# Kernel optimization log

Hardware: AMD Instinct MI355X
Metric: run time of the kernel (lower is better)

Reference implementation:

```python
import jax, jax.numpy as jnp
import numpy as np

IMG_W, IMG_H = 800, 800
OH, OW = 7, 7


def setup_inputs() -> dict:
    key = jax.random.key(0)
    k1, k2, k3 = jax.random.split(key, 3)
    feature_map = jax.random.normal(k1, (1, 256, 200, 200), dtype=jnp.float32)
    # boxes in image pixel coords, x1<=x2 and y1<=y2
    xs = jnp.sort(jax.random.uniform(k2, (1024, 2), dtype=jnp.float32) * (IMG_W - 1), axis=1)
    ys = jnp.sort(jax.random.uniform(k3, (1024, 2), dtype=jnp.float32) * (IMG_H - 1), axis=1)
    boxes = jnp.stack([xs[:, 0], ys[:, 0], xs[:, 1], ys[:, 1]], axis=1)
    return {"feature_map": feature_map, "boxes": boxes}


def reference(feature_map, boxes):
    # feature_map: [1, C, H, W]; boxes: [N, 4] (x1, y1, x2, y2) in image coords
    fm = feature_map[0]                      # [C, H, W]
    C, H, W = fm.shape
    scale = jnp.array([W / IMG_W, H / IMG_H, W / IMG_W, H / IMG_H], dtype=boxes.dtype)
    b = jnp.floor(boxes * scale).astype(jnp.int32)
    x1 = jnp.clip(b[:, 0], 0, W - 1)
    y1 = jnp.clip(b[:, 1], 0, H - 1)
    x2 = jnp.clip(b[:, 2] + 1, x1 + 1, W)    # exclusive end, clamped like torch slicing
    y2 = jnp.clip(b[:, 3] + 1, y1 + 1, H)
    rh = y2 - y1                             # [N]
    rw = x2 - x1
    # adaptive_avg_pool2d bin edges: start=floor(i*L/O), end=ceil((i+1)*L/O)
    i = jnp.arange(OH)
    j = jnp.arange(OW)
    rs = y1[:, None] + (i[None, :] * rh[:, None]) // OH                  # [N, OH]
    re = y1[:, None] + ((i[None, :] + 1) * rh[:, None] + OH - 1) // OH
    cs = x1[:, None] + (j[None, :] * rw[:, None]) // OW                  # [N, OW]
    ce = x1[:, None] + ((j[None, :] + 1) * rw[:, None] + OW - 1) // OW
    # integral image with zero row/col padding: ii[c, r, k] = sum fm[c, :r, :k]
    ii = jnp.pad(jnp.cumsum(jnp.cumsum(fm, axis=1), axis=2), ((0, 0), (1, 0), (1, 0)))

    def S(r, c):  # r: [N, OH], c: [N, OW] -> [N, C, OH, OW]
        return ii[:, r[:, :, None], c[:, None, :]].transpose(1, 0, 2, 3)

    total = S(re, ce) - S(rs, ce) - S(re, cs) + S(rs, cs)               # [N, C, OH, OW]
    area = ((re - rs)[:, :, None] * (ce - cs)[:, None, :]).astype(fm.dtype)  # [N, OH, OW]
    return total / area[:, None, :, :]
```

## Files before the change

### kernel.cpp

```cpp
#include <hip/hip_runtime.h>

#define C_CH  256
#define H_FM  200
#define W_FM  200
#define N_BOX 1024
#define OHp   7
#define OWp   7
#define NG    8
#define CG    32
#define WC    (W_FM * C_CH)
#define NCHUNK 25
#define CHROWS 8
#define GSTRIDE (H_FM * W_FM * CG)
#define HSTRIDE (W_FM * CG)
#define AUXG    (NCHUNK * HSTRIDE)


__global__ __launch_bounds__(256) void transpose_wscan_kernel(const float* __restrict__ fm,
                                                              float* __restrict__ T2) {
    __shared__ float tile[W_FM][CG + 1];
    __shared__ float tot[8][CG + 1];
    __shared__ float offE[8][CG + 1];
    const int t = threadIdx.x;
    const int h = blockIdx.x;
    const int g = blockIdx.y;
    const int c0 = g * CG;

    #pragma unroll
    for (int s = 0; s < 25; ++s) {
        int flat = s * 256 + t;
        int ci = flat / W_FM;
        int w  = flat - ci * W_FM;
        tile[w][ci] = fm[(size_t)(c0 + ci) * (H_FM * W_FM) + (size_t)h * W_FM + w];
    }
    __syncthreads();

    const int cg  = t & 31;
    const int chb = t >> 5;
    {
        float acc = 0.0f;
        #pragma unroll
        for (int s = 0; s < 25; ++s) {
            acc += tile[chb * 25 + s][cg];
            tile[chb * 25 + s][cg] = acc;
        }
        tot[chb][cg] = acc;
    }
    __syncthreads();

    {
        float off = 0.0f;
        #pragma unroll
        for (int k = 0; k < 8; ++k) {
            float v = tot[k][cg];
            if (k < chb) off += v;
        }
        offE[chb][cg] = off;
    }
    __syncthreads();

    float* dst = T2 + (size_t)g * GSTRIDE + (size_t)h * HSTRIDE;
    #pragma unroll
    for (int m = 0; m < 25; ++m) {
        int flat = m * 256 + t;
        int w  = flat >> 5;
        int cc = flat & 31;
        dst[flat] = tile[w][cc] + offE[w / 25][cc];
    }
}

__global__ __launch_bounds__(256) void colscan_chunk_kernel(float* __restrict__ T2,
                                                            float* __restrict__ aux2) {
    const int q4 = blockIdx.x * 256 + threadIdx.x;
    const int ch = blockIdx.y;
    const int g  = q4 / (HSTRIDE / 4);
    const int r4 = q4 - g * (HSTRIDE / 4);
    float4* p = (float4*)T2 + (size_t)g * (GSTRIDE / 4)
                            + (size_t)(ch * CHROWS) * (HSTRIDE / 4) + r4;
    float4 acc = make_float4(0.f, 0.f, 0.f, 0.f);
    #pragma unroll
    for (int k = 0; k < CHROWS; ++k) {
        float4 v = p[(size_t)k * (HSTRIDE / 4)];
        acc.x += v.x; acc.y += v.y; acc.z += v.z; acc.w += v.w;
        p[(size_t)k * (HSTRIDE / 4)] = acc;
    }
    ((float4*)aux2)[(size_t)g * (AUXG / 4) + (size_t)ch * (HSTRIDE / 4) + r4] = acc;
}

__global__ __launch_bounds__(256) void aux_scan_kernel(float* __restrict__ aux2) {
    const int idx = blockIdx.x * 256 + threadIdx.x;
    const int g   = idx / (HSTRIDE / 4);
    const int r4  = idx - g * (HSTRIDE / 4);
    float4* p = (float4*)aux2 + (size_t)g * (AUXG / 4) + r4;
    float4 acc = make_float4(0.f, 0.f, 0.f, 0.f);
    #pragma unroll
    for (int ch = 0; ch < NCHUNK; ++ch) {
        float4 v = p[(size_t)ch * (HSTRIDE / 4)];
        p[(size_t)ch * (HSTRIDE / 4)] = acc;
        acc.x += v.x; acc.y += v.y; acc.z += v.z; acc.w += v.w;
    }
}

__global__ __launch_bounds__(256) void pool5_kernel(const float* __restrict__ T2,
                                                    const float* __restrict__ aux2,
                                                    const float* __restrict__ boxes,
                                                    float* __restrict__ out) {
    __shared__ __align__(16) float lo[CG * 49];
    const int bx = blockIdx.x;
    const int n  = bx >> 3;
    const int g  = bx & 7;
    const int t  = threadIdx.x;
    const int cg = t & 31;
    const int islot = t >> 5;

    const float4 box = ((const float4*)boxes)[n];
    int b0 = (int)floorf(box.x * 0.25f);
    int b1 = (int)floorf(box.y * 0.25f);
    int b2 = (int)floorf(box.z * 0.25f);
    int b3 = (int)floorf(box.w * 0.25f);
    int x1 = min(max(b0, 0), W_FM - 1);
    int y1 = min(max(b1, 0), H_FM - 1);
    int x2 = min(max(b2 + 1, x1 + 1), W_FM);
    int y2 = min(max(b3 + 1, y1 + 1), H_FM);
    int rh = y2 - y1;
    int rw = x2 - x1;

    if (islot < OHp) {
        const int i  = islot;
        const int rt = y1 + (i * rh) / OHp;
        const int rb = y1 + ((i + 1) * rh + OHp - 1) / OHp;
        int colv[2 * OWp];
        #pragma unroll
        for (int j = 0; j < OWp; ++j) {
            colv[j]       = x1 + (j * rw) / OWp;
            colv[OWp + j] = x1 + ((j + 1) * rw + OWp - 1) / OWp;
        }
        const float* base = T2   + (size_t)g * GSTRIDE + cg;
        const float* abase = aux2 + (size_t)g * AUXG   + cg;
        const int ra  = max(rt - 1, 0) * W_FM;
        const int rbm = (rb - 1) * W_FM;
        const int ca  = (max(rt - 1, 0) >> 3) * W_FM;
        const int cb  = ((rb - 1) >> 3) * W_FM;
        float top[2 * OWp], bot[2 * OWp];
        #pragma unroll
        for (int k = 0; k < 2 * OWp; ++k) {
            const int kk = colv[k];
            const int ka = max(kk - 1, 0);
            float tv = base[(size_t)(ra  + ka) * CG] + abase[(size_t)(ca + ka) * CG];
            float bv = base[(size_t)(rbm + ka) * CG] + abase[(size_t)(cb + ka) * CG];
            top[k] = (rt > 0 && kk > 0) ? tv : 0.0f;
            bot[k] = (kk > 0)           ? bv : 0.0f;
        }
        const float rowspan = (float)(rb - rt);
        #pragma unroll
        for (int j = 0; j < OWp; ++j) {
            float total = (bot[OWp + j] - bot[j]) - (top[OWp + j] - top[j]);
            float area  = rowspan * (float)(colv[OWp + j] - colv[j]);
            lo[cg * 49 + i * OWp + j] = total / area;
        }
    }
    __syncthreads();

    float4* dst4 = (float4*)(out + (size_t)n * (C_CH * 49) + (size_t)g * (CG * 49));
    const float4* lo4 = (const float4*)lo;
    #pragma unroll
    for (int m = 0; m < 2; ++m) {
        int idx = m * 256 + t;
        if (idx < CG * 49 / 4) dst4[idx] = lo4[idx];
    }
}

__device__ __forceinline__ void box_edges(const float4 box, int i, int j,
                                          int& rs, int& re, int& cs, int& ce) {
    int b0 = (int)floorf(box.x * 0.25f);
    int b1 = (int)floorf(box.y * 0.25f);
    int b2 = (int)floorf(box.z * 0.25f);
    int b3 = (int)floorf(box.w * 0.25f);
    int x1 = min(max(b0, 0), W_FM - 1);
    int y1 = min(max(b1, 0), H_FM - 1);
    int x2 = min(max(b2 + 1, x1 + 1), W_FM);
    int y2 = min(max(b3 + 1, y1 + 1), H_FM);
    int rh = y2 - y1;
    int rw = x2 - x1;
    rs = y1 + (i * rh) / OHp;
    re = y1 + ((i + 1) * rh + OHp - 1) / OHp;
    cs = x1 + (j * rw) / OWp;
    ce = x1 + ((j + 1) * rw + OWp - 1) / OWp;
}

__global__ __launch_bounds__(256) void pool_direct_kernel(const float* __restrict__ fm,
                                                          const float* __restrict__ boxes,
                                                          float* __restrict__ out) {
    const int idx = blockIdx.x * 256 + threadIdx.x;
    const int j  = idx % OWp;
    const int t1 = idx / OWp;
    const int i  = t1 % OHp;
    const int t2 = t1 / OHp;
    const int c  = t2 % C_CH;
    const int n  = t2 / C_CH;

    const float4 box = ((const float4*)boxes)[n];
    int rs, re, cs, ce;
    box_edges(box, i, j, rs, re, cs, ce);

    const float* base = fm + (size_t)c * (H_FM * W_FM);
    float sum = 0.0f;
    for (int r = rs; r < re; ++r) {
        const float* rowp = base + (size_t)r * W_FM;
        for (int k = cs; k < ce; ++k) sum += rowp[k];
    }
    float area = (float)((re - rs) * (ce - cs));
    out[idx] = sum / area;
}

extern "C" void kernel_launch(void* const* d_in, const int* in_sizes, int n_in,
                              void* d_out, int out_size, void* d_ws, size_t ws_size,
                              hipStream_t stream) {
    const float* fm    = (const float*)d_in[0];
    const float* boxes = (const float*)d_in[1];
    float* out = (float*)d_out;

    const size_t tBytes   = (size_t)NG * GSTRIDE * sizeof(float);
    const size_t auxBytes = (size_t)NG * AUXG * sizeof(float);
    const int    total    = N_BOX * C_CH * OHp * OWp;
    const int    blocks   = total / 256;

    if (ws_size >= tBytes + auxBytes) {
        float* T2   = (float*)d_ws;
        float* aux2 = (float*)((char*)d_ws + tBytes);
        transpose_wscan_kernel<<<dim3(H_FM, NG), 256, 0, stream>>>(fm, T2);
        colscan_chunk_kernel<<<dim3(WC / 4 / 256, NCHUNK), 256, 0, stream>>>(T2, aux2);
        aux_scan_kernel<<<WC / 4 / 256, 256, 0, stream>>>(aux2);
        pool5_kernel<<<N_BOX * NG, 256, 0, stream>>>(T2, aux2, boxes, out);
    } else {
        pool_direct_kernel<<<blocks, 256, 0, stream>>>(fm, boxes, out);
    }
}
```

Measured before the change: 141.4 us.

## Fuse transpose, row scan and chunked column scan; stage pool corners in LDS

Merges the transpose/width-scan kernel with the chunked column-scan kernel. Each block walks 8 rows and carries running column sums in registers, so the extra read-modify-write pass over the integral buffer is gone. The pooling kernel now gathers all 14x14 corner values with vectorized loads into shared memory before combining them. The aux scan uses smaller blocks. The fused scan launches only 200 blocks with serialized row iterations, which may leave the GPU underoccupied.

```diff
diff --git a/kernel.cpp b/kernel.cpp
--- a/kernel.cpp
+++ b/kernel.cpp
@@ -16,79 +16,93 @@
 #define AUXG    (NCHUNK * HSTRIDE)
 
 
-__global__ __launch_bounds__(256) void transpose_wscan_kernel(const float* __restrict__ fm,
-                                                              float* __restrict__ T2) {
+__global__ __launch_bounds__(256) void fused_scan_kernel(const float* __restrict__ fm,
+                                                         float* __restrict__ T2,
+                                                         float* __restrict__ aux2) {
     __shared__ float tile[W_FM][CG + 1];
     __shared__ float tot[8][CG + 1];
     __shared__ float offE[8][CG + 1];
-    const int t = threadIdx.x;
-    const int h = blockIdx.x;
-    const int g = blockIdx.y;
-    const int c0 = g * CG;
-
-    #pragma unroll
-    for (int s = 0; s < 25; ++s) {
-        int flat = s * 256 + t;
-        int ci = flat / W_FM;
-        int w  = flat - ci * W_FM;
-        tile[w][ci] = fm[(size_t)(c0 + ci) * (H_FM * W_FM) + (size_t)h * W_FM + w];
-    }
-    __syncthreads();
-
+    const int t   = threadIdx.x;
+    const int chk = blockIdx.x;
+    const int g   = blockIdx.y;
+    const int c0  = g * CG;
+    const int h0  = chk * CHROWS;
     const int cg  = t & 31;
     const int chb = t >> 5;
-    {
-        float acc = 0.0f;
+
+    float4 acc[7];
+    #pragma unroll
+    for (int u = 0; u < 7; ++u) acc[u] = make_float4(0.f, 0.f, 0.f, 0.f);
+
+    const float* srcBase = fm + (size_t)c0 * (H_FM * W_FM);
+    float* dstBase = T2 + (size_t)g * GSTRIDE;
+
+    for (int hh = 0; hh < CHROWS; ++hh) {
+        const int h = h0 + hh;
+        const float* src = srcBase + (size_t)h * W_FM;
         #pragma unroll
-        for (int s = 0; s < 25; ++s) {
-            acc += tile[chb * 25 + s][cg];
-            tile[chb * 25 + s][cg] = acc;
-        }
-        tot[chb][cg] = acc;
-    }
-    __syncthreads();
-
-    {
-        float off = 0.0f;
+        for (int it = 0; it < 7; ++it) {
+            int item = it * 256 + t;
+            if (item < 1600) {
+                int ci = item / 50;
+                int w4 = item - ci * 50;
+                float4 v = *(const float4*)(src + (size_t)ci * (H_FM * W_FM) + w4 * 4);
+                tile[w4 * 4 + 0][ci] = v.x;
+                tile[w4 * 4 + 1][ci] = v.y;
+                tile[w4 * 4 + 2][ci] = v.z;
+                tile[w4 * 4 + 3][ci] = v.w;
+            }
+        }
+        __syncthreads();
+        {
+            float a = 0.f;
+            #pragma unroll
+            for (int s = 0; s < 25; ++s) {
+                a += tile[chb * 25 + s][cg];
+                tile[chb * 25 + s][cg] = a;
+            }
+            tot[chb][cg] = a;
+        }
+        __syncthreads();
+        {
+            float off = 0.f;
+            #pragma unroll
+            for (int k = 0; k < 8; ++k) {
+                float v = tot[k][cg];
+                if (k < chb) off += v;
+            }
+            offE[chb][cg] = off;
+        }
+        __syncthreads();
+        float* dst = dstBase + (size_t)h * HSTRIDE;
         #pragma unroll
-        for (int k = 0; k < 8; ++k) {
-            float v = tot[k][cg];
-            if (k < chb) off += v;
-        }
-        offE[chb][cg] = off;
-    }
-    __syncthreads();
-
-    float* dst = T2 + (size_t)g * GSTRIDE + (size_t)h * HSTRIDE;
-    #pragma unroll
-    for (int m = 0; m < 25; ++m) {
-        int flat = m * 256 + t;
-        int w  = flat >> 5;
-        int cc = flat & 31;
-        dst[flat] = tile[w][cc] + offE[w / 25][cc];
-    }
-}
-
-__global__ __launch_bounds__(256) void colscan_chunk_kernel(float* __restrict__ T2,
-                                                            float* __restrict__ aux2) {
-    const int q4 = blockIdx.x * 256 + threadIdx.x;
-    const int ch = blockIdx.y;
-    const int g  = q4 / (HSTRIDE / 4);
-    const int r4 = q4 - g * (HSTRIDE / 4);
-    float4* p = (float4*)T2 + (size_t)g * (GSTRIDE / 4)
-                            + (size_t)(ch * CHROWS) * (HSTRIDE / 4) + r4;
-    float4 acc = make_float4(0.f, 0.f, 0.f, 0.f);
-    #pragma unroll
-    for (int k = 0; k < CHROWS; ++k) {
-        float4 v = p[(size_t)k * (HSTRIDE / 4)];
-        acc.x += v.x; acc.y += v.y; acc.z += v.z; acc.w += v.w;
-        p[(size_t)k * (HSTRIDE / 4)] = acc;
-    }
-    ((float4*)aux2)[(size_t)g * (AUXG / 4) + (size_t)ch * (HSTRIDE / 4) + r4] = acc;
-}
-
-__global__ __launch_bounds__(256) void aux_scan_kernel(float* __restrict__ aux2) {
-    const int idx = blockIdx.x * 256 + threadIdx.x;
+        for (int it = 0; it < 7; ++it) {
+            int f4 = it * 256 + t;
+            if (f4 < 1600) {
+                int w  = f4 >> 3;
+                int cc = (f4 & 7) * 4;
+                int wb = w / 25;
+                float4 v;
+                v.x = tile[w][cc + 0] + offE[wb][cc + 0] + acc[it].x;
+                v.y = tile[w][cc + 1] + offE[wb][cc + 1] + acc[it].y;
+                v.z = tile[w][cc + 2] + offE[wb][cc + 2] + acc[it].z;
+                v.w = tile[w][cc + 3] + offE[wb][cc + 3] + acc[it].w;
+                acc[it] = v;
+                *(float4*)(dst + (size_t)f4 * 4) = v;
+            }
+        }
+        __syncthreads();
+    }
+    float* adst = aux2 + (size_t)g * AUXG + (size_t)chk * HSTRIDE;
+    #pragma unroll
+    for (int it = 0; it < 7; ++it) {
+        int f4 = it * 256 + t;
+        if (f4 < 1600) *(float4*)(adst + (size_t)f4 * 4) = acc[it];
+    }
+}
+
+__global__ __launch_bounds__(64) void aux_scan_kernel(float* __restrict__ aux2) {
+    const int idx = blockIdx.x * 64 + threadIdx.x;
     const int g   = idx / (HSTRIDE / 4);
     const int r4  = idx - g * (HSTRIDE / 4);
     float4* p = (float4*)aux2 + (size_t)g * (AUXG / 4) + r4;
@@ -101,17 +115,16 @@
     }
 }
 
-__global__ __launch_bounds__(256) void pool5_kernel(const float* __restrict__ T2,
+__global__ __launch_bounds__(256) void pool6_kernel(const float* __restrict__ T2,
                                                     const float* __restrict__ aux2,
                                                     const float* __restrict__ boxes,
                                                     float* __restrict__ out) {
+    __shared__ __align__(16) float grid[196][36];
     __shared__ __align__(16) float lo[CG * 49];
     const int bx = blockIdx.x;
     const int n  = bx >> 3;
     const int g  = bx & 7;
     const int t  = threadIdx.x;
-    const int cg = t & 31;
-    const int islot = t >> 5;
 
     const float4 box = ((const float4*)boxes)[n];
     int b0 = (int)floorf(box.x * 0.25f);
@@ -125,38 +138,54 @@
     int rh = y2 - y1;
     int rw = x2 - x1;
 
-    if (islot < OHp) {
-        const int i  = islot;
-        const int rt = y1 + (i * rh) / OHp;
-        const int rb = y1 + ((i + 1) * rh + OHp - 1) / OHp;
-        int colv[2 * OWp];
+    {
+        const int c4 = t & 7;
+        const int p0 = t >> 3;
+        const float* Tg = T2   + (size_t)g * GSTRIDE + c4 * 4;
+        const float* Ag = aux2 + (size_t)g * AUXG   + c4 * 4;
         #pragma unroll
-        for (int j = 0; j < OWp; ++j) {
-            colv[j]       = x1 + (j * rw) / OWp;
-            colv[OWp + j] = x1 + ((j + 1) * rw + OWp - 1) / OWp;
-        }
-        const float* base = T2   + (size_t)g * GSTRIDE + cg;
-        const float* abase = aux2 + (size_t)g * AUXG   + cg;
-        const int ra  = max(rt - 1, 0) * W_FM;
-        const int rbm = (rb - 1) * W_FM;
-        const int ca  = (max(rt - 1, 0) >> 3) * W_FM;
-        const int cb  = ((rb - 1) >> 3) * W_FM;
-        float top[2 * OWp], bot[2 * OWp];
-        #pragma unroll
-        for (int k = 0; k < 2 * OWp; ++k) {
-            const int kk = colv[k];
-            const int ka = max(kk - 1, 0);
-            float tv = base[(size_t)(ra  + ka) * CG] + abase[(size_t)(ca + ka) * CG];
-            float bv = base[(size_t)(rbm + ka) * CG] + abase[(size_t)(cb + ka) * CG];
-            top[k] = (rt > 0 && kk > 0) ? tv : 0.0f;
-            bot[k] = (kk > 0)           ? bv : 0.0f;
-        }
-        const float rowspan = (float)(rb - rt);
-        #pragma unroll
-        for (int j = 0; j < OWp; ++j) {
-            float total = (bot[OWp + j] - bot[j]) - (top[OWp + j] - top[j]);
-            float area  = rowspan * (float)(colv[OWp + j] - colv[j]);
-            lo[cg * 49 + i * OWp + j] = total / area;
+        for (int it = 0; it < 7; ++it) {
+            int pos = it * 32 + p0;
+            if (pos < 196) {
+                int ri = pos / 14;
+                int ci = pos - ri * 14;
+                int r = (ri < 7) ? (y1 + (ri * rh) / OHp)
+                                 : (y1 + ((ri - 6) * rh + OHp - 1) / OHp);
+                int k = (ci < 7) ? (x1 + (ci * rw) / OWp)
+                                 : (x1 + ((ci - 6) * rw + OWp - 1) / OWp);
+                float4 v = make_float4(0.f, 0.f, 0.f, 0.f);
+                if (r > 0 && k > 0) {
+                    float4 tv = *(const float4*)(Tg + ((size_t)(r - 1) * W_FM + (k - 1)) * CG);
+                    float4 av = *(const float4*)(Ag + ((size_t)((r - 1) >> 3) * W_FM + (k - 1)) * CG);
+                    v.x = tv.x + av.x; v.y = tv.y + av.y;
+                    v.z = tv.z + av.z; v.w = tv.w + av.w;
+                }
+                *(float4*)&grid[pos][c4 * 4] = v;
+            }
+        }
+    }
+    __syncthreads();
+
+    {
+        const int cg = t & 31;
+        const int islot = t >> 5;
+        if (islot < OHp) {
+            const int i  = islot;
+            const int rt = y1 + (i * rh) / OHp;
+            const int rb = y1 + ((i + 1) * rh + OHp - 1) / OHp;
+            const float rowspan = (float)(rb - rt);
+            #pragma unroll
+            for (int j = 0; j < OWp; ++j) {
+                const int csj = x1 + (j * rw) / OWp;
+                const int cej = x1 + ((j + 1) * rw + OWp - 1) / OWp;
+                float a = grid[(7 + i) * 14 + 7 + j][cg];
+                float b = grid[i * 14 + 7 + j][cg];
+                float c = grid[(7 + i) * 14 + j][cg];
+                float d = grid[i * 14 + j][cg];
+                float total = (a - b) - (c - d);
+                float area  = rowspan * (float)(cej - csj);
+                lo[cg * 49 + i * OWp + j] = total / area;
+            }
         }
     }
     __syncthreads();
@@ -228,10 +257,9 @@
     if (ws_size >= tBytes + auxBytes) {
         float* T2   = (float*)d_ws;
         float* aux2 = (float*)((char*)d_ws + tBytes);
-        transpose_wscan_kernel<<<dim3(H_FM, NG), 256, 0, stream>>>(fm, T2);
-        colscan_chunk_kernel<<<dim3(WC / 4 / 256, NCHUNK), 256, 0, stream>>>(T2, aux2);
-        aux_scan_kernel<<<WC / 4 / 256, 256, 0, stream>>>(aux2);
-        pool5_kernel<<<N_BOX * NG, 256, 0, stream>>>(T2, aux2, boxes, out);
+        fused_scan_kernel<<<dim3(NCHUNK, NG), 256, 0, stream>>>(fm, T2, aux2);
+        aux_scan_kernel<<<WC / 4 / 64, 64, 0, stream>>>(aux2);
+        pool6_kernel<<<N_BOX * NG, 256, 0, stream>>>(T2, aux2, boxes, out);
     } else {
         pool_direct_kernel<<<blocks, 256, 0, stream>>>(fm, boxes, out);
     }
```

Measured after the change: 160.8 us. +13.7%, slower.

## Gather integral-image corners with float4 loads into shared grid before pooling

Applied to the files above, without the earlier changes.

The pooling kernel now computes the 14 row and 14 column bin edges once into shared memory. All 256 threads then gather the 196 corner values per channel group with vectorized float4 loads into a shared grid, where previously 224 threads each issued scalar loads. The per-bin differences are then read from shared memory. The aux scan launch is also reshaped to 64-thread blocks, giving more blocks for a small kernel. The cost is extra shared memory (about 28KB per block) and an additional barrier, which may reduce occupancy.

```diff
diff --git a/kernel.cpp b/kernel.cpp
--- a/kernel.cpp
+++ b/kernel.cpp
@@ -87,8 +87,8 @@
     ((float4*)aux2)[(size_t)g * (AUXG / 4) + (size_t)ch * (HSTRIDE / 4) + r4] = acc;
 }
 
-__global__ __launch_bounds__(256) void aux_scan_kernel(float* __restrict__ aux2) {
-    const int idx = blockIdx.x * 256 + threadIdx.x;
+__global__ __launch_bounds__(64) void aux_scan_kernel(float* __restrict__ aux2) {
+    const int idx = blockIdx.x * 64 + threadIdx.x;
     const int g   = idx / (HSTRIDE / 4);
     const int r4  = idx - g * (HSTRIDE / 4);
     float4* p = (float4*)aux2 + (size_t)g * (AUXG / 4) + r4;
@@ -101,17 +101,18 @@
     }
 }
 
-__global__ __launch_bounds__(256) void pool5_kernel(const float* __restrict__ T2,
+__global__ __launch_bounds__(256) void pool7_kernel(const float* __restrict__ T2,
                                                     const float* __restrict__ aux2,
                                                     const float* __restrict__ boxes,
                                                     float* __restrict__ out) {
+    __shared__ __align__(16) float grid[196][36];
     __shared__ __align__(16) float lo[CG * 49];
+    __shared__ int er[14];
+    __shared__ int ec[14];
     const int bx = blockIdx.x;
     const int n  = bx >> 3;
     const int g  = bx & 7;
     const int t  = threadIdx.x;
-    const int cg = t & 31;
-    const int islot = t >> 5;
 
     const float4 box = ((const float4*)boxes)[n];
     int b0 = (int)floorf(box.x * 0.25f);
@@ -125,38 +126,58 @@
     int rh = y2 - y1;
     int rw = x2 - x1;
 
-    if (islot < OHp) {
-        const int i  = islot;
-        const int rt = y1 + (i * rh) / OHp;
-        const int rb = y1 + ((i + 1) * rh + OHp - 1) / OHp;
-        int colv[2 * OWp];
+    if (t < 14) {
+        er[t] = (t < 7) ? (y1 + (t * rh) / OHp)
+                        : (y1 + ((t - 6) * rh + OHp - 1) / OHp);
+    } else if (t >= 64 && t < 78) {
+        int u = t - 64;
+        ec[u] = (u < 7) ? (x1 + (u * rw) / OWp)
+                        : (x1 + ((u - 6) * rw + OWp - 1) / OWp);
+    }
+    __syncthreads();
+
+    {
+        const int c4 = t & 7;
+        const int p0 = t >> 3;
+        const float* Tg = T2   + (size_t)g * GSTRIDE + c4 * 4;
+        const float* Ag = aux2 + (size_t)g * AUXG   + c4 * 4;
         #pragma unroll
-        for (int j = 0; j < OWp; ++j) {
-            colv[j]       = x1 + (j * rw) / OWp;
-            colv[OWp + j] = x1 + ((j + 1) * rw + OWp - 1) / OWp;
-        }
-        const float* base = T2   + (size_t)g * GSTRIDE + cg;
-        const float* abase = aux2 + (size_t)g * AUXG   + cg;
-        const int ra  = max(rt - 1, 0) * W_FM;
-        const int rbm = (rb - 1) * W_FM;
-        const int ca  = (max(rt - 1, 0) >> 3) * W_FM;
-        const int cb  = ((rb - 1) >> 3) * W_FM;
-        float top[2 * OWp], bot[2 * OWp];
-        #pragma unroll
-        for (int k = 0; k < 2 * OWp; ++k) {
-            const int kk = colv[k];
-            const int ka = max(kk - 1, 0);
-            float tv = base[(size_t)(ra  + ka) * CG] + abase[(size_t)(ca + ka) * CG];
-            float bv = base[(size_t)(rbm + ka) * CG] + abase[(size_t)(cb + ka) * CG];
-            top[k] = (rt > 0 && kk > 0) ? tv : 0.0f;
-            bot[k] = (kk > 0)           ? bv : 0.0f;
-        }
-        const float rowspan = (float)(rb - rt);
-        #pragma unroll
-        for (int j = 0; j < OWp; ++j) {
-            float total = (bot[OWp + j] - bot[j]) - (top[OWp + j] - top[j]);
-            float area  = rowspan * (float)(colv[OWp + j] - colv[j]);
-            lo[cg * 49 + i * OWp + j] = total / area;
+        for (int it = 0; it < 7; ++it) {
+            int pos = it * 32 + p0;
+            if (pos < 196) {
+                int ri = pos / 14;
+                int ci = pos - ri * 14;
+                int r = er[ri];
+                int k = ec[ci];
+                float4 v = make_float4(0.f, 0.f, 0.f, 0.f);
+                if (r > 0 && k > 0) {
+                    float4 tv = *(const float4*)(Tg + ((size_t)(r - 1) * W_FM + (k - 1)) * CG);
+                    float4 av = *(const float4*)(Ag + ((size_t)((r - 1) >> 3) * W_FM + (k - 1)) * CG);
+                    v.x = tv.x + av.x; v.y = tv.y + av.y;
+                    v.z = tv.z + av.z; v.w = tv.w + av.w;
+                }
+                *(float4*)&grid[pos][c4 * 4] = v;
+            }
+        }
+    }
+    __syncthreads();
+
+    {
+        const int cg = t & 31;
+        const int islot = t >> 5;
+        if (islot < OHp) {
+            const int i  = islot;
+            const float rowspan = (float)(er[7 + i] - er[i]);
+            #pragma unroll
+            for (int j = 0; j < OWp; ++j) {
+                float a = grid[(7 + i) * 14 + 7 + j][cg];
+                float b = grid[i * 14 + 7 + j][cg];
+                float c = grid[(7 + i) * 14 + j][cg];
+                float d = grid[i * 14 + j][cg];
+                float total = (a - b) - (c - d);
+                float area  = rowspan * (float)(ec[7 + j] - ec[j]);
+                lo[cg * 49 + i * OWp + j] = total / area;
+            }
         }
     }
     __syncthreads();
@@ -230,8 +251,8 @@
         float* aux2 = (float*)((char*)d_ws + tBytes);
         transpose_wscan_kernel<<<dim3(H_FM, NG), 256, 0, stream>>>(fm, T2);
         colscan_chunk_kernel<<<dim3(WC / 4 / 256, NCHUNK), 256, 0, stream>>>(T2, aux2);
-        aux_scan_kernel<<<WC / 4 / 256, 256, 0, stream>>>(aux2);
-        pool5_kernel<<<N_BOX * NG, 256, 0, stream>>>(T2, aux2, boxes, out);
+        aux_scan_kernel<<<WC / 4 / 64, 64, 0, stream>>>(aux2);
+        pool7_kernel<<<N_BOX * NG, 256, 0, stream>>>(T2, aux2, boxes, out);
     } else {
         pool_direct_kernel<<<blocks, 256, 0, stream>>>(fm, boxes, out);
     }
```

Result: slower. 146.1 us (+3.3%).
